# Performance work log

Hardware: AMD Instinct MI355X
Metric: run time of the kernel (lower is better)

Reference implementation:

```python
import jax, jax.numpy as jnp
import numpy as np

EPS_NORM = 1e-6
EPS_Q = 1e-5


def rmsnorm(x, g):
    ms = jnp.mean(x * x, axis=-1, keepdims=True)
    return x * jax.lax.rsqrt(ms + EPS_NORM) * g


def bitlinear(x, w, g):
    # RMSNorm -> absmax int8 activation quant -> absmean ternary weight quant -> matmul -> rescale
    xn = rmsnorm(x, g)
    x_scale = jnp.maximum(jnp.max(jnp.abs(xn), axis=-1, keepdims=True), EPS_Q)
    xq = jnp.clip(jnp.round(xn * 127.0 / x_scale), -128.0, 127.0)  # STE irrelevant in fwd
    w_scale = jnp.maximum(jnp.mean(jnp.abs(w)), EPS_Q)
    wq = jnp.clip(jnp.round(w / w_scale), -1.0, 1.0)
    out = jnp.einsum('btd,od->bto', xq, wq)
    return out * (w_scale * x_scale / 127.0)


def rotate_half(x):
    d = x.shape[-1] // 2
    return jnp.concatenate([-x[..., d:], x[..., :d]], axis=-1)


def apply_rope(x, cos, sin):
    # x: [B, H, T, D]; cos/sin: [T, D]
    return x * cos[None, None] + rotate_half(x) * sin[None, None]


def setup_inputs() -> dict:
    key = jax.random.key(0)
    ks = jax.random.split(key, 12)
    B, T, D, H, KV = 2, 2048, 2048, 32, 8
    hd = D // H
    bound = 1.0 / np.sqrt(D)  # ~ kaiming_uniform fan_in
    inp = {
        'x': jax.random.normal(ks[0], (B, T, D), jnp.float32),
        'cos': jax.random.uniform(ks[1], (T, hd), jnp.float32),
        'sin': jax.random.uniform(ks[2], (T, hd), jnp.float32),
        'wq': jax.random.uniform(ks[3], (H * hd, D), jnp.float32, -bound, bound),
        'wk': jax.random.uniform(ks[4], (KV * hd, D), jnp.float32, -bound, bound),
        'wv': jax.random.uniform(ks[5], (KV * hd, D), jnp.float32, -bound, bound),
        'wo': jax.random.uniform(ks[6], (D, H * hd), jnp.float32, -bound, bound),
        'gq': jnp.ones((D,), jnp.float32),
        'gk': jnp.ones((D,), jnp.float32),
        'gv': jnp.ones((D,), jnp.float32),
        'go': jnp.ones((H * hd,), jnp.float32),
    }
    return inp


def reference(x, cos, sin, wq, wk, wv, wo, gq, gk, gv, go):
    B, T, D = x.shape
    H, KV = 32, 8
    hd = D // H
    n_rep = H // KV

    q = bitlinear(x, wq, gq).reshape(B, T, H, hd).transpose(0, 2, 1, 3)   # [B,H,T,hd]
    k = bitlinear(x, wk, gk).reshape(B, T, KV, hd).transpose(0, 2, 1, 3)  # [B,KV,T,hd]
    v = bitlinear(x, wv, gv).reshape(B, T, KV, hd).transpose(0, 2, 1, 3)

    q = apply_rope(q, cos, sin)
    k = apply_rope(k, cos, sin)

    # GQA repeat_interleave on head dim
    k = jnp.repeat(k, n_rep, axis=1)  # [B,H,T,hd]
    v = jnp.repeat(v, n_rep, axis=1)

    scale = 1.0 / np.sqrt(hd)
    scores = jnp.einsum('bhqd,bhkd->bhqk', q, k) * scale
    causal = jnp.tril(jnp.ones((T, T), bool))
    scores = jnp.where(causal, scores, jnp.finfo(scores.dtype).min)
    attn = jax.nn.softmax(scores, axis=-1)
    out = jnp.einsum('bhqk,bhkd->bhqd', attn, v)
    out = out.transpose(0, 2, 1, 3).reshape(B, T, H * hd)
    return bitlinear(out, wo, go)
```

## Files before the change

### kernel.cpp

```cpp
#include <hip/hip_runtime.h>
#include <stdint.h>

constexpr int B   = 2;
constexpr int T   = 2048;
constexpr int D   = 2048;
constexpr int H   = 32;
constexpr int KVH = 8;
constexpr int HD  = 64;
constexpr int R   = B * T;
constexpr int OKV = KVH * HD;

using bf16x8 = __attribute__((ext_vector_type(8))) __bf16;
using f32x4  = __attribute__((ext_vector_type(4))) float;
using i32x4  = __attribute__((ext_vector_type(4))) int;

__device__ inline float fast_exp2(float x) {
#if __has_builtin(__builtin_amdgcn_exp2f)
    return __builtin_amdgcn_exp2f(x);
#else
    return exp2f(x);
#endif
}

__device__ inline uint16_t f2bf(float f) {
    uint32_t u = __float_as_uint(f);
    u += 0x7fff + ((u >> 16) & 1);
    return (uint16_t)(u >> 16);
}

__device__ inline uint32_t pack_bf16(float a, float b) {
#if __has_builtin(__builtin_amdgcn_cvt_pk_bf16_f32)
    union { __attribute__((ext_vector_type(2))) __bf16 v; uint32_t u; } r;
    r.v = __builtin_amdgcn_cvt_pk_bf16_f32(a, b);
    return r.u;
#else
    return (uint32_t)f2bf(a) | ((uint32_t)f2bf(b) << 16);
#endif
}

__device__ inline void async16(const void* g, void* l) {
    __builtin_amdgcn_global_load_lds((const __attribute__((address_space(1))) unsigned int*)g,
                                     (__attribute__((address_space(3))) unsigned int*)l,
                                     16, 0, 0);
}

__global__ void absmean4_kernel(const float* __restrict__ w0, const float* __restrict__ w1,
                                const float* __restrict__ w2, const float* __restrict__ w3,
                                double* __restrict__ sums) {
    __shared__ float red[256];
    const float* ws[4] = {w0, w1, w2, w3};
    const int ns[4] = {D * D, OKV * D, OKV * D, D * D};
    int wi = blockIdx.y;
    const float* w = ws[wi];
    int n = ns[wi];
    int tid = threadIdx.x;
    float s = 0.f;
    for (int i = blockIdx.x * 256 + tid; i < n; i += gridDim.x * 256)
        s += fabsf(w[i]);
    red[tid] = s;
    __syncthreads();
    for (int st = 128; st > 0; st >>= 1) {
        if (tid < st) red[tid] += red[tid + st];
        __syncthreads();
    }
    if (tid == 0) atomicAdd(&sums[wi], (double)red[0]);
}

__global__ void quantw4_kernel(const float* __restrict__ w0, const float* __restrict__ w1,
                               const float* __restrict__ w2, const float* __restrict__ w3,
                               int8_t* __restrict__ o0, int8_t* __restrict__ o1,
                               int8_t* __restrict__ o2, int8_t* __restrict__ o3,
                               const double* __restrict__ sums) {
    const float* ws[4] = {w0, w1, w2, w3};
    int8_t* os[4] = {o0, o1, o2, o3};
    const int ns[4] = {D * D, OKV * D, OKV * D, D * D};
    int wi = blockIdx.y;
    const float* w = ws[wi];
    int8_t* o = os[wi];
    int n = ns[wi];
    float wsc = fmaxf((float)(sums[wi] / (double)n), 1e-5f);
    for (int i = blockIdx.x * 256 + threadIdx.x; i < n; i += gridDim.x * 256) {
        float q = rintf(w[i] / wsc);
        q = fminf(fmaxf(q, -1.f), 1.f);
        o[i] = (int8_t)q;
    }
}

__global__ __launch_bounds__(256) void rmsq3_kernel(const float* __restrict__ X,
        const float* __restrict__ g0, const float* __restrict__ g1, const float* __restrict__ g2,
        int8_t* __restrict__ o0, int8_t* __restrict__ o1, int8_t* __restrict__ o2,
        float* __restrict__ s0, float* __restrict__ s1, float* __restrict__ s2) {
    __shared__ float red[256];
    int row = blockIdx.x, tid = threadIdx.x;
    const float* xr = X + (size_t)row * D;
    float xv[8];
    float ss = 0.f;
#pragma unroll
    for (int i = 0; i < 8; i++) { xv[i] = xr[tid + 256 * i]; ss += xv[i] * xv[i]; }
    red[tid] = ss;
    __syncthreads();
    for (int st = 128; st > 0; st >>= 1) {
        if (tid < st) red[tid] += red[tid + st];
        __syncthreads();
    }
    float rstd = 1.0f / sqrtf(red[0] / (float)D + 1e-6f);

    const float* gs[3] = {g0, g1, g2};
    int8_t* os[3] = {o0, o1, o2};
    float* sc[3] = {s0, s1, s2};
#pragma unroll
    for (int v = 0; v < 3; v++) {
        float xn[8];
        float amax = 0.f;
#pragma unroll
        for (int i = 0; i < 8; i++) {
            xn[i] = xv[i] * rstd * gs[v][tid + 256 * i];
            amax = fmaxf(amax, fabsf(xn[i]));
        }
        __syncthreads();
        red[tid] = amax;
        __syncthreads();
        for (int st = 128; st > 0; st >>= 1) {
            if (tid < st) red[tid] = fmaxf(red[tid], red[tid + st]);
            __syncthreads();
        }
        float xsv = fmaxf(red[0], 1e-5f);
        float q127 = 127.0f / xsv;
#pragma unroll
        for (int i = 0; i < 8; i++) {
            float q = rintf(xn[i] * q127);
            q = fminf(fmaxf(q, -128.f), 127.f);
            os[v][(size_t)row * D + tid + 256 * i] = (int8_t)q;
        }
        if (tid == 0) sc[v][row] = xsv;
    }
}

__global__ void rmsq_kernel(const float* __restrict__ X, const float* __restrict__ g,
                            int8_t* __restrict__ Xq, float* __restrict__ xs_out) {
    __shared__ float red[256];
    int row = blockIdx.x;
    int tid = threadIdx.x;
    const float* xr = X + (size_t)row * D;

    float ss = 0.f;
    for (int i = tid; i < D; i += 256) { float v = xr[i]; ss += v * v; }
    red[tid] = ss;
    __syncthreads();
    for (int st = 128; st > 0; st >>= 1) {
        if (tid < st) red[tid] += red[tid + st];
        __syncthreads();
    }
    float ms = red[0] / (float)D;
    float rstd = 1.0f / sqrtf(ms + 1e-6f);
    __syncthreads();

    float amax = 0.f;
    for (int i = tid; i < D; i += 256) {
        float xn = xr[i] * rstd * g[i];
        amax = fmaxf(amax, fabsf(xn));
    }
    red[tid] = amax;
    __syncthreads();
    for (int st = 128; st > 0; st >>= 1) {
        if (tid < st) red[tid] = fmaxf(red[tid], red[tid + st]);
        __syncthreads();
    }
    float xs = fmaxf(red[0], 1e-5f);

    for (int i = tid; i < D; i += 256) {
        float xn = xr[i] * rstd * g[i];
        float q = rintf(xn * 127.0f / xs);
        q = fminf(fmaxf(q, -128.f), 127.f);
        Xq[(size_t)row * D + i] = (int8_t)q;
    }
    if (tid == 0) xs_out[row] = xs;
}

template<int BN, int MODE>
__global__ __launch_bounds__(256) void gemm_i8_mfma(const int8_t* __restrict__ Xq,
                                                    const int8_t* __restrict__ W8,
                                                    void* __restrict__ outp,
                                                    const float* __restrict__ xs,
                                                    const double* __restrict__ wsum, int wi,
                                                    int nw, int O,
                                                    const float* __restrict__ cs,
                                                    const float* __restrict__ sn) {
    constexpr int NT = BN / 16;
    __shared__ __align__(16) uint8_t As[128 * 128];
    __shared__ __align__(16) uint8_t Bs[BN * 128];

    const int tid  = threadIdx.x;
    const int lane = tid & 63;
    const int wv   = tid >> 6;
    const int n    = lane & 15, quad = lane >> 4;
    const int row0 = blockIdx.y * 128;
    const int col0 = blockIdx.x * BN;

    i32x4 acc[2][NT] = {};

    for (int k0 = 0; k0 < D; k0 += 128) {
        __syncthreads();
#pragma unroll
        for (int j = 0; j < 4; j++) {
            int p = wv * 256 + j * 64 + lane;
            int r = p >> 3, s = p & 7;
            int c = s ^ (r & 7);
            async16(Xq + (size_t)(row0 + r) * D + k0 + c * 16,
                    &As[(size_t)(wv * 256 + j * 64) * 16]);
        }
#pragma unroll
        for (int j = 0; j < BN / 32; j++) {
            int p = wv * (BN * 2) + j * 64 + lane;
            int r = p >> 3, s = p & 7;
            int c = s ^ (r & 7);
            async16(W8 + (size_t)(col0 + r) * D + k0 + c * 16,
                    &Bs[(size_t)(wv * (BN * 2) + j * 64) * 16]);
        }
        __syncthreads();
#pragma unroll
        for (int t = 0; t < 2; t++) {
            i32x4 af[2], bfr[NT];
#pragma unroll
            for (int mt = 0; mt < 2; mt++) {
                int r = wv * 32 + mt * 16 + n;
                af[mt] = *(const i32x4*)&As[r * 128 + (((t * 4 + quad) ^ (r & 7)) * 16)];
            }
#pragma unroll
            for (int nt = 0; nt < NT; nt++) {
                int r = nt * 16 + n;
                bfr[nt] = *(const i32x4*)&Bs[r * 128 + (((t * 4 + quad) ^ (r & 7)) * 16)];
            }
#pragma unroll
            for (int mt = 0; mt < 2; mt++)
#pragma unroll
                for (int nt = 0; nt < NT; nt++)
                    acc[mt][nt] = __builtin_amdgcn_mfma_i32_16x16x64_i8(af[mt], bfr[nt], acc[mt][nt], 0, 0, 0);
        }
    }
    float w = fmaxf((float)(wsum[wi] / (double)nw), 1e-5f);
#pragma unroll
    for (int mt = 0; mt < 2; mt++) {
#pragma unroll
        for (int r2 = 0; r2 < 4; r2++) {
            int row = row0 + wv * 32 + mt * 16 + quad * 4 + r2;
            float f = w * xs[row] * (1.0f / 127.0f);
            if (MODE == 0) {
                float* out = (float*)outp;
#pragma unroll
                for (int nt = 0; nt < NT; nt++)
                    out[(size_t)row * O + col0 + nt * 16 + n] = (float)acc[mt][nt][r2] * f;
            } else {
                uint16_t* out = (uint16_t*)outp;
                int t = row & (T - 1);
#pragma unroll
                for (int nt = 0; nt < NT; nt++) {
                    if ((nt & 3) >= 2) continue;
                    int i = (nt * 16 + n) & 63;
                    float a  = (float)acc[mt][nt][r2] * f;
                    float bb = (float)acc[mt][nt + 2][r2] * f;
                    float c0 = cs[t * HD + i],      s0 = sn[t * HD + i];
                    float c1 = cs[t * HD + i + 32], s1 = sn[t * HD + i + 32];
                    out[(size_t)row * O + col0 + nt * 16 + n]       = f2bf(a * c0 - bb * s0);
                    out[(size_t)row * O + col0 + (nt + 2) * 16 + n] = f2bf(bb * c1 + a * s1);
                }
            }
        }
    }
}

__global__ __launch_bounds__(256) void vtrans_kernel(const float* __restrict__ vb,
                                                     uint16_t* __restrict__ vt) {
    __shared__ float tile[64][65];
    int t0 = blockIdx.x * 64;
    int hb = blockIdx.y;
    int b = hb >> 3, kvh = hb & 7;
    int tid = threadIdx.x;
    int r = tid >> 2, cg = (tid & 3) * 16;
#pragma unroll
    for (int j = 0; j < 4; j++) {
        float4 v4 = *(const float4*)(vb + (size_t)(b * T + t0 + r) * OKV + kvh * HD + cg + j * 4);
        tile[r][cg + j * 4 + 0] = v4.x;
        tile[r][cg + j * 4 + 1] = v4.y;
        tile[r][cg + j * 4 + 2] = v4.z;
        tile[r][cg + j * 4 + 3] = v4.w;
    }
    __syncthreads();
    int d = tid >> 2, tg = (tid & 3) * 16;
    uint16_t pk[16];
#pragma unroll
    for (int j = 0; j < 16; j++) pk[j] = f2bf(tile[tg + j][d]);
    *(uint4*)(vt + ((size_t)hb * 64 + d) * T + t0 + tg)     = *(uint4*)&pk[0];
    *(uint4*)(vt + ((size_t)hb * 64 + d) * T + t0 + tg + 8) = *(uint4*)&pk[8];
}

__global__ __launch_bounds__(512, 4) void attn_mfma_kernel(const uint16_t* __restrict__ qh,
                                                           const uint16_t* __restrict__ kh,
                                                           const uint16_t* __restrict__ vt,
                                                           float* __restrict__ out) {
    __shared__ __align__(16) uint16_t KsB[2][64 * 64];
    __shared__ __align__(16) uint16_t VtB[2][64 * 64];
    __shared__ __align__(16) uint16_t Pw[8][16 * 72];

    const int tid  = threadIdx.x;
    const int lane = tid & 63;
    const int wv   = tid >> 6;
    const int p = blockIdx.x, h = blockIdx.y, b = blockIdx.z;
    const int kvh = h >> 2;
    const int n = lane & 15, quad = lane >> 4;
    const float SC = 0.125f * 1.44269504089f;
    const float DEFER = 44.3614f;

    int q_lo[2] = { p * 128 + wv * 16, (15 - p) * 128 + wv * 16 };

    bf16x8 qf[2][2];
#pragma unroll
    for (int i = 0; i < 2; i++) {
        const uint16_t* qp = qh + (size_t)(b * T + q_lo[i] + n) * D + h * HD + quad * 8;
        qf[i][0] = *(const bf16x8*)(qp);
        qf[i][1] = *(const bf16x8*)(qp + 32);
    }

    f32x4 o[2][4] = {};
    float ls[2] = { 0.f, 0.f };
    float m[2] = { -INFINITY, -INFINITY };

    const uint16_t* kbase = kh + (size_t)b * T * OKV + kvh * HD;
    const uint16_t* vbase = vt + (size_t)(b * KVH + kvh) * 64 * T;

    const int nch = 32 - 2 * p;

    {
        int r = tid >> 3, sl = tid & 7;
        int c = sl ^ (r & 7);
        async16(kbase + (size_t)r * OKV + c * 8, &KsB[0][wv * 512]);
        async16(vbase + (size_t)r * T + c * 8,   &VtB[0][wv * 512]);
    }
    __syncthreads();

    for (int ch = 0; ch < nch; ch++) {
        const int cur = ch & 1;
        if (ch + 1 < nch) {
            const int t1 = (ch + 1) * 64;
            int r = tid >> 3, sl = tid & 7;
            int c = sl ^ (r & 7);
            async16(kbase + (size_t)(t1 + r) * OKV + c * 8, &KsB[cur ^ 1][wv * 512]);
            async16(vbase + (size_t)r * T + t1 + c * 8,     &VtB[cur ^ 1][wv * 512]);
        }
        const int t0 = ch * 64;
        const uint16_t* Ks = KsB[cur];
        const uint16_t* Vs = VtB[cur];

#pragma unroll
        for (int i = 0; i < 2; i++) {
            if (t0 > q_lo[i] + 15) continue;
            f32x4 sv[4] = {};
            __builtin_amdgcn_s_setprio(1);
#pragma unroll
            for (int ks = 0; ks < 2; ks++)
#pragma unroll
                for (int mt = 0; mt < 4; mt++) {
                    int r = mt * 16 + n;
                    bf16x8 kfr = *(const bf16x8*)&Ks[r * 64 + (((ks * 4 + quad) ^ (n & 7)) * 8)];
                    sv[mt] = __builtin_amdgcn_mfma_f32_16x16x32_bf16(kfr, qf[i][ks], sv[mt], 0, 0, 0);
                }
            __builtin_amdgcn_s_setprio(0);

            const int qg = q_lo[i] + n;
            const bool diag = (t0 + 63 > q_lo[i]);
            float mloc = -INFINITY;
#pragma unroll
            for (int mt = 0; mt < 4; mt++)
#pragma unroll
                for (int r2 = 0; r2 < 4; r2++) {
                    float x = sv[mt][r2];
                    if (diag) {
                        int kg = t0 + mt * 16 + quad * 4 + r2;
                        x = (kg > qg) ? -INFINITY : x;
                        sv[mt][r2] = x;
                    }
                    mloc = fmaxf(mloc, x);
                }
            mloc = fmaxf(mloc, __shfl_xor(mloc, 16));
            mloc = fmaxf(mloc, __shfl_xor(mloc, 32));
            bool upd = (mloc > m[i] + DEFER);
            if (__ballot(upd)) {
                float mnew = fmaxf(m[i], mloc);
                float corr = fast_exp2((m[i] - mnew) * SC);
                m[i] = mnew;
#pragma unroll
                for (int mt = 0; mt < 4; mt++)
#pragma unroll
                    for (int r2 = 0; r2 < 4; r2++) o[i][mt][r2] *= corr;
                ls[i] *= corr;
            }
            float msc = m[i] * SC;
#pragma unroll
            for (int mt = 0; mt < 4; mt++) {
                float pv[4];
#pragma unroll
                for (int r2 = 0; r2 < 4; r2++)
                    pv[r2] = fast_exp2(__builtin_fmaf(sv[mt][r2], SC, -msc));
                ls[i] += (pv[0] + pv[1]) + (pv[2] + pv[3]);
                uint2 w2;
                w2.x = pack_bf16(pv[0], pv[1]);
                w2.y = pack_bf16(pv[2], pv[3]);
                *(uint2*)&Pw[wv][n * 72 + mt * 16 + quad * 4] = w2;
            }
            __builtin_amdgcn_s_setprio(1);
#pragma unroll
            for (int ks = 0; ks < 2; ks++) {
                bf16x8 pf = *(const bf16x8*)&Pw[wv][n * 72 + ks * 32 + quad * 8];
#pragma unroll
                for (int mt = 0; mt < 4; mt++) {
                    int r = mt * 16 + n;
                    bf16x8 vfr = *(const bf16x8*)&Vs[r * 64 + (((ks * 4 + quad) ^ (n & 7)) * 8)];
                    o[i][mt] = __builtin_amdgcn_mfma_f32_16x16x32_bf16(vfr, pf, o[i][mt], 0, 0, 0);
                }
            }
            __builtin_amdgcn_s_setprio(0);
        }
        __syncthreads();
    }

#pragma unroll
    for (int i = 0; i < 2; i++) {
        int qg = q_lo[i] + n;
        float l = ls[i];
        l += __shfl_xor(l, 16);
        l += __shfl_xor(l, 32);
        float inv = 1.0f / l;
#pragma unroll
        for (int mt = 0; mt < 4; mt++) {
            f32x4 ov;
#pragma unroll
            for (int r2 = 0; r2 < 4; r2++) ov[r2] = o[i][mt][r2] * inv;
            *(f32x4*)(out + (size_t)(b * T + qg) * D + h * HD + mt * 16 + quad * 4) = ov;
        }
    }
}

extern "C" void kernel_launch(void* const* d_in, const int* in_sizes, int n_in,
                              void* d_out, int out_size, void* d_ws, size_t ws_size,
                              hipStream_t stream) {
    const float* x   = (const float*)d_in[0];
    const float* cs  = (const float*)d_in[1];
    const float* sn  = (const float*)d_in[2];
    const float* wq  = (const float*)d_in[3];
    const float* wk  = (const float*)d_in[4];
    const float* wv  = (const float*)d_in[5];
    const float* wo  = (const float*)d_in[6];
    const float* gq  = (const float*)d_in[7];
    const float* gk  = (const float*)d_in[8];
    const float* gv  = (const float*)d_in[9];
    const float* go  = (const float*)d_in[10];
    float* out = (float*)d_out;

    uint8_t* w = (uint8_t*)d_ws;
    double* wsum  = (double*)w;
    float* xs     = (float*)(w + 256);
    size_t off = 256 + 4 * (size_t)R * 4;
    int8_t* Wq8 = (int8_t*)(w + off); off += (size_t)D * D;
    int8_t* Wk8 = (int8_t*)(w + off); off += (size_t)OKV * D;
    int8_t* Wv8 = (int8_t*)(w + off); off += (size_t)OKV * D;
    int8_t* Wo8 = (int8_t*)(w + off); off += (size_t)D * D;
    int8_t* Xq_q = (int8_t*)(w + off); off += (size_t)R * D;
    int8_t* Xq_k = (int8_t*)(w + off); off += (size_t)R * D;
    int8_t* Xq_v = (int8_t*)(w + off); off += (size_t)R * D;
    float* ab = (float*)(w + off); off += (size_t)R * D * 4;
    float* vb = (float*)(w + off); off += (size_t)R * OKV * 4;
    uint16_t* qhb = (uint16_t*)(w + off); off += (size_t)R * D * 2;
    uint16_t* khb = (uint16_t*)Xq_v;
    uint16_t* vtb = (uint16_t*)Xq_k;
    int8_t*   Aq8 = Xq_q;

    (void)hipMemsetAsync(wsum, 0, 64, stream);

    absmean4_kernel<<<dim3(256, 4), 256, 0, stream>>>(wq, wk, wv, wo, wsum);
    quantw4_kernel<<<dim3(1024, 4), 256, 0, stream>>>(wq, wk, wv, wo, Wq8, Wk8, Wv8, Wo8, wsum);

    rmsq3_kernel<<<R, 256, 0, stream>>>(x, gq, gk, gv, Xq_q, Xq_k, Xq_v,
                                        xs + 0 * R, xs + 1 * R, xs + 2 * R);

    gemm_i8_mfma<128, 1><<<dim3(D / 128, R / 128), 256, 0, stream>>>(
        Xq_q, Wq8, qhb, xs + 0 * R, wsum, 0, D * D, D, cs, sn);
    gemm_i8_mfma<64, 0><<<dim3(OKV / 64, R / 128), 256, 0, stream>>>(
        Xq_v, Wv8, vb, xs + 2 * R, wsum, 2, OKV * D, OKV, cs, sn);
    gemm_i8_mfma<64, 1><<<dim3(OKV / 64, R / 128), 256, 0, stream>>>(
        Xq_k, Wk8, khb, xs + 1 * R, wsum, 1, OKV * D, OKV, cs, sn);

    vtrans_kernel<<<dim3(T / 64, B * KVH), 256, 0, stream>>>(vb, vtb);

    attn_mfma_kernel<<<dim3(8, H, B), 512, 0, stream>>>(qhb, khb, vtb, ab);

    rmsq_kernel<<<R, 256, 0, stream>>>(ab, go, Aq8, xs + 3 * R);
    gemm_i8_mfma<128, 0><<<dim3(D / 128, R / 128), 256, 0, stream>>>(
        Aq8, Wo8, out, xs + 3 * R, wsum, 3, D * D, D, cs, sn);
}
```

Before: 371.2 us.

## Split attention into one query tile per block and cache rows in rmsq

The attention kernel drops the paired causal-balanced scheme, where each block handled tiles p and 15-p. It now launches 16 query tiles per head, each with its own block, and raises the occupancy hint from 4 to 6 blocks per CU. The aim is fewer registers per thread (one set of accumulators instead of two) and more blocks in flight, at the cost of uneven block run times and K/V tiles being loaded twice for the pairs that used to share them. Separately, rmsq_kernel keeps each row's values in registers, so it reads X once instead of three times and multiplies by a precomputed reciprocal instead of dividing.

Result: slower. 413.4 us (+11.4%).

```diff
diff --git a/kernel.cpp b/kernel.cpp
--- a/kernel.cpp
+++ b/kernel.cpp
@@ -136,30 +136,33 @@
     }
 }
 
-__global__ void rmsq_kernel(const float* __restrict__ X, const float* __restrict__ g,
-                            int8_t* __restrict__ Xq, float* __restrict__ xs_out) {
+__global__ __launch_bounds__(256) void rmsq_kernel(const float* __restrict__ X,
+                                                   const float* __restrict__ g,
+                                                   int8_t* __restrict__ Xq,
+                                                   float* __restrict__ xs_out) {
     __shared__ float red[256];
-    int row = blockIdx.x;
-    int tid = threadIdx.x;
+    int row = blockIdx.x, tid = threadIdx.x;
     const float* xr = X + (size_t)row * D;
-
+    float xv[8];
     float ss = 0.f;
-    for (int i = tid; i < D; i += 256) { float v = xr[i]; ss += v * v; }
+#pragma unroll
+    for (int i = 0; i < 8; i++) { xv[i] = xr[tid + 256 * i]; ss += xv[i] * xv[i]; }
     red[tid] = ss;
     __syncthreads();
     for (int st = 128; st > 0; st >>= 1) {
         if (tid < st) red[tid] += red[tid + st];
         __syncthreads();
     }
-    float ms = red[0] / (float)D;
-    float rstd = 1.0f / sqrtf(ms + 1e-6f);
-    __syncthreads();
-
+    float rstd = 1.0f / sqrtf(red[0] / (float)D + 1e-6f);
+
+    float xn[8];
     float amax = 0.f;
-    for (int i = tid; i < D; i += 256) {
-        float xn = xr[i] * rstd * g[i];
-        amax = fmaxf(amax, fabsf(xn));
-    }
+#pragma unroll
+    for (int i = 0; i < 8; i++) {
+        xn[i] = xv[i] * rstd * g[tid + 256 * i];
+        amax = fmaxf(amax, fabsf(xn[i]));
+    }
+    __syncthreads();
     red[tid] = amax;
     __syncthreads();
     for (int st = 128; st > 0; st >>= 1) {
@@ -167,12 +170,12 @@
         __syncthreads();
     }
     float xs = fmaxf(red[0], 1e-5f);
-
-    for (int i = tid; i < D; i += 256) {
-        float xn = xr[i] * rstd * g[i];
-        float q = rintf(xn * 127.0f / xs);
+    float q127 = 127.0f / xs;
+#pragma unroll
+    for (int i = 0; i < 8; i++) {
+        float q = rintf(xn[i] * q127);
         q = fminf(fmaxf(q, -128.f), 127.f);
-        Xq[(size_t)row * D + i] = (int8_t)q;
+        Xq[(size_t)row * D + tid + 256 * i] = (int8_t)q;
     }
     if (tid == 0) xs_out[row] = xs;
 }
@@ -294,7 +297,7 @@
     *(uint4*)(vt + ((size_t)hb * 64 + d) * T + t0 + tg + 8) = *(uint4*)&pk[8];
 }
 
-__global__ __launch_bounds__(512, 4) void attn_mfma_kernel(const uint16_t* __restrict__ qh,
+__global__ __launch_bounds__(512, 6) void attn_mfma_kernel(const uint16_t* __restrict__ qh,
                                                            const uint16_t* __restrict__ kh,
                                                            const uint16_t* __restrict__ vt,
                                                            float* __restrict__ out) {
@@ -305,30 +308,29 @@
     const int tid  = threadIdx.x;
     const int lane = tid & 63;
     const int wv   = tid >> 6;
-    const int p = blockIdx.x, h = blockIdx.y, b = blockIdx.z;
+    const int s = blockIdx.x, h = blockIdx.y, b = blockIdx.z;
     const int kvh = h >> 2;
     const int n = lane & 15, quad = lane >> 4;
     const float SC = 0.125f * 1.44269504089f;
     const float DEFER = 44.3614f;
 
-    int q_lo[2] = { p * 128 + wv * 16, (15 - p) * 128 + wv * 16 };
-
-    bf16x8 qf[2][2];
-#pragma unroll
-    for (int i = 0; i < 2; i++) {
-        const uint16_t* qp = qh + (size_t)(b * T + q_lo[i] + n) * D + h * HD + quad * 8;
-        qf[i][0] = *(const bf16x8*)(qp);
-        qf[i][1] = *(const bf16x8*)(qp + 32);
-    }
-
-    f32x4 o[2][4] = {};
-    float ls[2] = { 0.f, 0.f };
-    float m[2] = { -INFINITY, -INFINITY };
+    const int q_lo = s * 128 + wv * 16;
+
+    bf16x8 qf[2];
+    {
+        const uint16_t* qp = qh + (size_t)(b * T + q_lo + n) * D + h * HD + quad * 8;
+        qf[0] = *(const bf16x8*)(qp);
+        qf[1] = *(const bf16x8*)(qp + 32);
+    }
+
+    f32x4 o[4] = {};
+    float ls = 0.f;
+    float m = -INFINITY;
 
     const uint16_t* kbase = kh + (size_t)b * T * OKV + kvh * HD;
     const uint16_t* vbase = vt + (size_t)(b * KVH + kvh) * 64 * T;
 
-    const int nch = 32 - 2 * p;
+    const int nch = 2 * s + 2;
 
     {
         int r = tid >> 3, sl = tid & 7;
@@ -351,9 +353,7 @@
         const uint16_t* Ks = KsB[cur];
         const uint16_t* Vs = VtB[cur];
 
-#pragma unroll
-        for (int i = 0; i < 2; i++) {
-            if (t0 > q_lo[i] + 15) continue;
+        if (t0 <= q_lo + 15) {
             f32x4 sv[4] = {};
             __builtin_amdgcn_s_setprio(1);
 #pragma unroll
@@ -362,12 +362,12 @@
                 for (int mt = 0; mt < 4; mt++) {
                     int r = mt * 16 + n;
                     bf16x8 kfr = *(const bf16x8*)&Ks[r * 64 + (((ks * 4 + quad) ^ (n & 7)) * 8)];
-                    sv[mt] = __builtin_amdgcn_mfma_f32_16x16x32_bf16(kfr, qf[i][ks], sv[mt], 0, 0, 0);
+                    sv[mt] = __builtin_amdgcn_mfma_f32_16x16x32_bf16(kfr, qf[ks], sv[mt], 0, 0, 0);
                 }
             __builtin_amdgcn_s_setprio(0);
 
-            const int qg = q_lo[i] + n;
-            const bool diag = (t0 + 63 > q_lo[i]);
+            const int qg = q_lo + n;
+            const bool diag = (t0 + 63 > q_lo);
             float mloc = -INFINITY;
 #pragma unroll
             for (int mt = 0; mt < 4; mt++)
@@ -383,25 +383,25 @@
                 }
             mloc = fmaxf(mloc, __shfl_xor(mloc, 16));
             mloc = fmaxf(mloc, __shfl_xor(mloc, 32));
-            bool upd = (mloc > m[i] + DEFER);
+            bool upd = (mloc > m + DEFER);
             if (__ballot(upd)) {
-                float mnew = fmaxf(m[i], mloc);
-                float corr = fast_exp2((m[i] - mnew) * SC);
-                m[i] = mnew;
+                float mnew = fmaxf(m, mloc);
+                float corr = fast_exp2((m - mnew) * SC);
+                m = mnew;
 #pragma unroll
                 for (int mt = 0; mt < 4; mt++)
 #pragma unroll
-                    for (int r2 = 0; r2 < 4; r2++) o[i][mt][r2] *= corr;
-                ls[i] *= corr;
-            }
-            float msc = m[i] * SC;
+                    for (int r2 = 0; r2 < 4; r2++) o[mt][r2] *= corr;
+                ls *= corr;
+            }
+            float msc = m * SC;
 #pragma unroll
             for (int mt = 0; mt < 4; mt++) {
                 float pv[4];
 #pragma unroll
                 for (int r2 = 0; r2 < 4; r2++)
                     pv[r2] = fast_exp2(__builtin_fmaf(sv[mt][r2], SC, -msc));
-                ls[i] += (pv[0] + pv[1]) + (pv[2] + pv[3]);
+                ls += (pv[0] + pv[1]) + (pv[2] + pv[3]);
                 uint2 w2;
                 w2.x = pack_bf16(pv[0], pv[1]);
                 w2.y = pack_bf16(pv[2], pv[3]);
@@ -415,7 +415,7 @@
                 for (int mt = 0; mt < 4; mt++) {
                     int r = mt * 16 + n;
                     bf16x8 vfr = *(const bf16x8*)&Vs[r * 64 + (((ks * 4 + quad) ^ (n & 7)) * 8)];
-                    o[i][mt] = __builtin_amdgcn_mfma_f32_16x16x32_bf16(vfr, pf, o[i][mt], 0, 0, 0);
+                    o[mt] = __builtin_amdgcn_mfma_f32_16x16x32_bf16(vfr, pf, o[mt], 0, 0, 0);
                 }
             }
             __builtin_amdgcn_s_setprio(0);
@@ -423,10 +423,9 @@
         __syncthreads();
     }
 
-#pragma unroll
-    for (int i = 0; i < 2; i++) {
-        int qg = q_lo[i] + n;
-        float l = ls[i];
+    {
+        int qg = q_lo + n;
+        float l = ls;
         l += __shfl_xor(l, 16);
         l += __shfl_xor(l, 32);
         float inv = 1.0f / l;
@@ -434,7 +433,7 @@
         for (int mt = 0; mt < 4; mt++) {
             f32x4 ov;
 #pragma unroll
-            for (int r2 = 0; r2 < 4; r2++) ov[r2] = o[i][mt][r2] * inv;
+            for (int r2 = 0; r2 < 4; r2++) ov[r2] = o[mt][r2] * inv;
             *(f32x4*)(out + (size_t)(b * T + qg) * D + h * HD + mt * 16 + quad * 4) = ov;
         }
     }
@@ -491,7 +490,7 @@
 
     vtrans_kernel<<<dim3(T / 64, B * KVH), 256, 0, stream>>>(vb, vtb);
 
-    attn_mfma_kernel<<<dim3(8, H, B), 512, 0, stream>>>(qhb, khb, vtb, ab);
+    attn_mfma_kernel<<<dim3(16, H, B), 512, 0, stream>>>(qhb, khb, vtb, ab);
 
     rmsq_kernel<<<R, 256, 0, stream>>>(ab, go, Aq8, xs + 3 * R);
     gemm_i8_mfma<128, 0><<<dim3(D / 128, R / 128), 256, 0, stream>>>(
```

## Fuse V transpose into V GEMM epilogue and cache rows in rmsq registers

Applied to the files above, without the earlier changes.

Adds a GEMM epilogue mode that writes V already scaled, converted to bf16 and transposed into the [b,kvh,d,t] layout, so the separate vtrans kernel and the fp32 V intermediate are no longer needed. The output-projection rmsq kernel now keeps each row's values in registers across its three passes instead of reloading from global memory. The attention kernel's launch bound occupancy hint is raised from 4 to 6, which may force register spills.

After: 445.6 us. 1.2x slower.

```diff
diff --git a/kernel.cpp b/kernel.cpp
--- a/kernel.cpp
+++ b/kernel.cpp
@@ -136,30 +136,33 @@
     }
 }
 
-__global__ void rmsq_kernel(const float* __restrict__ X, const float* __restrict__ g,
-                            int8_t* __restrict__ Xq, float* __restrict__ xs_out) {
+__global__ __launch_bounds__(256) void rmsq_kernel(const float* __restrict__ X,
+                                                   const float* __restrict__ g,
+                                                   int8_t* __restrict__ Xq,
+                                                   float* __restrict__ xs_out) {
     __shared__ float red[256];
-    int row = blockIdx.x;
-    int tid = threadIdx.x;
+    int row = blockIdx.x, tid = threadIdx.x;
     const float* xr = X + (size_t)row * D;
-
+    float xv[8];
     float ss = 0.f;
-    for (int i = tid; i < D; i += 256) { float v = xr[i]; ss += v * v; }
+#pragma unroll
+    for (int i = 0; i < 8; i++) { xv[i] = xr[tid + 256 * i]; ss += xv[i] * xv[i]; }
     red[tid] = ss;
     __syncthreads();
     for (int st = 128; st > 0; st >>= 1) {
         if (tid < st) red[tid] += red[tid + st];
         __syncthreads();
     }
-    float ms = red[0] / (float)D;
-    float rstd = 1.0f / sqrtf(ms + 1e-6f);
-    __syncthreads();
-
+    float rstd = 1.0f / sqrtf(red[0] / (float)D + 1e-6f);
+
+    float xn[8];
     float amax = 0.f;
-    for (int i = tid; i < D; i += 256) {
-        float xn = xr[i] * rstd * g[i];
-        amax = fmaxf(amax, fabsf(xn));
-    }
+#pragma unroll
+    for (int i = 0; i < 8; i++) {
+        xn[i] = xv[i] * rstd * g[tid + 256 * i];
+        amax = fmaxf(amax, fabsf(xn[i]));
+    }
+    __syncthreads();
     red[tid] = amax;
     __syncthreads();
     for (int st = 128; st > 0; st >>= 1) {
@@ -167,12 +170,12 @@
         __syncthreads();
     }
     float xs = fmaxf(red[0], 1e-5f);
-
-    for (int i = tid; i < D; i += 256) {
-        float xn = xr[i] * rstd * g[i];
-        float q = rintf(xn * 127.0f / xs);
+    float q127 = 127.0f / xs;
+#pragma unroll
+    for (int i = 0; i < 8; i++) {
+        float q = rintf(xn[i] * q127);
         q = fminf(fmaxf(q, -128.f), 127.f);
-        Xq[(size_t)row * D + i] = (int8_t)q;
+        Xq[(size_t)row * D + tid + 256 * i] = (int8_t)q;
     }
     if (tid == 0) xs_out[row] = xs;
 }
@@ -241,6 +244,26 @@
     float w = fmaxf((float)(wsum[wi] / (double)nw), 1e-5f);
 #pragma unroll
     for (int mt = 0; mt < 2; mt++) {
+        if (MODE == 2) {
+            int rowb = row0 + wv * 32 + mt * 16 + quad * 4;
+            int bb = rowb >> 11;
+            int tb = rowb & (T - 1);
+            float fr[4];
+#pragma unroll
+            for (int r2 = 0; r2 < 4; r2++)
+                fr[r2] = w * xs[rowb + r2] * (1.0f / 127.0f);
+            uint16_t* o16 = (uint16_t*)outp;
+#pragma unroll
+            for (int nt = 0; nt < NT; nt++) {
+                int col = col0 + nt * 16 + n;
+                int kvh = col >> 6, d = col & 63;
+                uint2 w2;
+                w2.x = pack_bf16((float)acc[mt][nt][0] * fr[0], (float)acc[mt][nt][1] * fr[1]);
+                w2.y = pack_bf16((float)acc[mt][nt][2] * fr[2], (float)acc[mt][nt][3] * fr[3]);
+                *(uint2*)(o16 + ((size_t)(bb * KVH + kvh) * 64 + d) * T + tb) = w2;
+            }
+            continue;
+        }
 #pragma unroll
         for (int r2 = 0; r2 < 4; r2++) {
             int row = row0 + wv * 32 + mt * 16 + quad * 4 + r2;
@@ -269,32 +292,7 @@
     }
 }
 
-__global__ __launch_bounds__(256) void vtrans_kernel(const float* __restrict__ vb,
-                                                     uint16_t* __restrict__ vt) {
-    __shared__ float tile[64][65];
-    int t0 = blockIdx.x * 64;
-    int hb = blockIdx.y;
-    int b = hb >> 3, kvh = hb & 7;
-    int tid = threadIdx.x;
-    int r = tid >> 2, cg = (tid & 3) * 16;
-#pragma unroll
-    for (int j = 0; j < 4; j++) {
-        float4 v4 = *(const float4*)(vb + (size_t)(b * T + t0 + r) * OKV + kvh * HD + cg + j * 4);
-        tile[r][cg + j * 4 + 0] = v4.x;
-        tile[r][cg + j * 4 + 1] = v4.y;
-        tile[r][cg + j * 4 + 2] = v4.z;
-        tile[r][cg + j * 4 + 3] = v4.w;
-    }
-    __syncthreads();
-    int d = tid >> 2, tg = (tid & 3) * 16;
-    uint16_t pk[16];
-#pragma unroll
-    for (int j = 0; j < 16; j++) pk[j] = f2bf(tile[tg + j][d]);
-    *(uint4*)(vt + ((size_t)hb * 64 + d) * T + t0 + tg)     = *(uint4*)&pk[0];
-    *(uint4*)(vt + ((size_t)hb * 64 + d) * T + t0 + tg + 8) = *(uint4*)&pk[8];
-}
-
-__global__ __launch_bounds__(512, 4) void attn_mfma_kernel(const uint16_t* __restrict__ qh,
+__global__ __launch_bounds__(512, 6) void attn_mfma_kernel(const uint16_t* __restrict__ qh,
                                                            const uint16_t* __restrict__ kh,
                                                            const uint16_t* __restrict__ vt,
                                                            float* __restrict__ out) {
@@ -471,7 +469,7 @@
     float* vb = (float*)(w + off); off += (size_t)R * OKV * 4;
     uint16_t* qhb = (uint16_t*)(w + off); off += (size_t)R * D * 2;
     uint16_t* khb = (uint16_t*)Xq_v;
-    uint16_t* vtb = (uint16_t*)Xq_k;
+    uint16_t* vtb = (uint16_t*)vb;
     int8_t*   Aq8 = Xq_q;
 
     (void)hipMemsetAsync(wsum, 0, 64, stream);
@@ -484,12 +482,10 @@
 
     gemm_i8_mfma<128, 1><<<dim3(D / 128, R / 128), 256, 0, stream>>>(
         Xq_q, Wq8, qhb, xs + 0 * R, wsum, 0, D * D, D, cs, sn);
-    gemm_i8_mfma<64, 0><<<dim3(OKV / 64, R / 128), 256, 0, stream>>>(
-        Xq_v, Wv8, vb, xs + 2 * R, wsum, 2, OKV * D, OKV, cs, sn);
+    gemm_i8_mfma<64, 2><<<dim3(OKV / 64, R / 128), 256, 0, stream>>>(
+        Xq_v, Wv8, vtb, xs + 2 * R, wsum, 2, OKV * D, OKV, cs, sn);
     gemm_i8_mfma<64, 1><<<dim3(OKV / 64, R / 128), 256, 0, stream>>>(
         Xq_k, Wk8, khb, xs + 1 * R, wsum, 1, OKV * D, OKV, cs, sn);
-
-    vtrans_kernel<<<dim3(T / 64, B * KVH), 256, 0, stream>>>(vb, vtb);
 
     attn_mfma_kernel<<<dim3(8, H, B), 512, 0, stream>>>(qhb, khb, vtb, ab);
 
```
